# Kernel tuning notes

Measured on AMD Instinct MI355X. Metric: run time of the kernel, lower is better.

The kernel has to match this reference:

```python
import jax, jax.numpy as jnp
import numpy as np

SEQ_LEN = 256
VOCAB = 50000
EMBED = 300
PROJ = 200
ATT = 200
CLS = 3
B = 128


def setup_inputs() -> dict:
    key = jax.random.key(0)
    ks = jax.random.split(key, 16)
    s = lambda d: 1.0 / np.sqrt(d)
    return {
        "x1": jax.random.randint(ks[0], (B, SEQ_LEN), 0, VOCAB, dtype=jnp.int32),
        "x2": jax.random.randint(ks[1], (B, SEQ_LEN), 0, VOCAB, dtype=jnp.int32),
        "emb": jax.random.normal(ks[2], (VOCAB, EMBED), jnp.float32),
        # intra-attention forward_product FC (shared for x1/x2 via AUTO_REUSE)
        "Wi": jax.random.normal(ks[3], (EMBED, ATT), jnp.float32) * s(EMBED),
        "bi": jnp.zeros((ATT,), jnp.float32),
        "b_dist": jax.random.normal(ks[4], (1,), jnp.float32) * 0.1,
        # embed-scope projection (input is concat[x, xp] -> 2*EMBED), linear
        "Wp": jax.random.normal(ks[5], (2 * EMBED, PROJ), jnp.float32) * s(2 * EMBED),
        "bp": jnp.zeros((PROJ,), jnp.float32),
        # attent forward_product FC (shared)
        "Wa": jax.random.normal(ks[6], (PROJ, ATT), jnp.float32) * s(PROJ),
        "ba": jnp.zeros((ATT,), jnp.float32),
        # compare FC (shared, dim = input dim = 2*PROJ)
        "Wc": jax.random.normal(ks[7], (2 * PROJ, 2 * PROJ), jnp.float32) * s(2 * PROJ),
        "bc": jnp.zeros((2 * PROJ,), jnp.float32),
        # aggregate FC -> class logits (linear)
        "Wg": jax.random.normal(ks[8], (4 * PROJ, CLS), jnp.float32) * s(4 * PROJ),
        "bg": jnp.zeros((CLS,), jnp.float32),
    }


def _seq_mask(x):
    # tf.count_nonzero + tf.sequence_mask -> [B, L, 1] float mask
    size = jnp.sum((x != 0).astype(jnp.float32), axis=1)  # [B]
    m = (jnp.arange(SEQ_LEN)[None, :] < size[:, None]).astype(jnp.float32)
    return m[:, :, None]


def _intra(x, Wi, bi, b_dist):
    # forward_product on (x, x): relu FC then bilinear product -> [B, L, L]
    f = jax.nn.relu(x @ Wi + bi)
    att = jnp.einsum("bid,bjd->bij", f, f)
    idx = jnp.arange(SEQ_LEN)
    dist = jnp.abs(idx[None, :] - idx[:, None])
    bias = b_dist[0] * (dist >= 10).astype(jnp.float32)  # [L, L]
    xp = jnp.einsum("bik,bkj->bij", jax.nn.softmax(att + bias[None], axis=2), x)
    return jnp.concatenate([x, xp], axis=2)  # [B, L, 2*EMBED]


def reference(x1, x2, emb, Wi, bi, b_dist, Wp, bp, Wa, ba, Wc, bc, Wg, bg):
    mask1, mask2 = _seq_mask(x1), _seq_mask(x2)  # [B, L, 1]

    # embedding lookup with L2-normalized table
    emb_n = emb / jnp.linalg.norm(emb, axis=1, keepdims=True)
    e1, e2 = emb_n[x1], emb_n[x2]  # [B, L, EMBED]

    # intra-attention (distance-biased self alignment), doubles feature dim
    h1 = _intra(e1, Wi, bi, b_dist)
    h2 = _intra(e2, Wi, bi, b_dist)

    # linear projection to PROJ
    p1 = h1 @ Wp + bp  # [B, L, PROJ]
    p2 = h2 @ Wp + bp

    # attent: forward_product sim + mask + dual-axis softmax alignments
    a1 = jax.nn.relu(p1 @ Wa + ba)
    a2 = jax.nn.relu(p2 @ Wa + ba)
    sim = jnp.einsum("bid,bjd->bij", a1, a2)  # [B, L, L]
    sim = sim * (mask1 * jnp.swapaxes(mask2, 1, 2))
    alpha = jnp.einsum("bki,bkj->bij", jax.nn.softmax(sim, axis=1), p1)
    beta = jnp.einsum("bik,bkj->bij", jax.nn.softmax(sim, axis=2), p2)

    # compare (shared relu FC)
    v1 = jax.nn.relu(jnp.concatenate([p1, beta], 2) @ Wc + bc)
    v2 = jax.nn.relu(jnp.concatenate([p2, alpha], 2) @ Wc + bc)

    # aggregate: masked sum pooling + linear classifier
    v1 = jnp.sum(v1 * mask1, axis=1)  # [B, 2*PROJ]
    v2 = jnp.sum(v2 * mask2, axis=1)
    return jnp.concatenate([v1, v2], 1) @ Wg + bg  # [B, CLS]
```

## Files before the change

kernel.cpp:

```cpp
#include <hip/hip_runtime.h>
#include <math.h>

#define LSEQ 256
#define NB   128

typedef unsigned short u16;
typedef unsigned int   u32;
typedef __attribute__((ext_vector_type(8))) short bf16x8;
typedef __attribute__((ext_vector_type(4))) float f32x4;

static __device__ __forceinline__ u16 f2bf(float x) {
    union { float f; u32 u; } v; v.f = x;
    const u32 r = v.u + 0x7fffu + ((v.u >> 16) & 1u);
    return (u16)(r >> 16);
}
static __device__ __forceinline__ u32 cvt_pk(float lo, float hi) {
    u32 r; asm("v_cvt_pk_bf16_f32 %0, %1, %2" : "=v"(r) : "v"(lo), "v"(hi));
    return r;
}
static __device__ __forceinline__ u16 f2bf_fast(float x) {
    u32 r; asm("v_cvt_pk_bf16_f32 %0, %1, %1" : "=v"(r) : "v"(x));
    return (u16)r;
}
static __device__ __forceinline__ void glds16(const u16* src, u16* dst) {
    __builtin_amdgcn_global_load_lds(
        (const __attribute__((address_space(1))) u32*)src,
        (__attribute__((address_space(3))) u32*)dst, 16, 0, 0);
}
static __device__ __forceinline__ void bar_lgkm() {
    asm volatile("s_waitcnt lgkmcnt(0)" ::: "memory");
    __builtin_amdgcn_s_barrier();
}

template<int EPI, bool BIAS, bool RELU>
__global__ __launch_bounds__(512)
void gemm(const u16* __restrict__ A, int lda,
          const u16* __restrict__ B, int ldb,
          u16* __restrict__ C, int ldc,
          const float* __restrict__ bias, int Nbias,
          float* __restrict__ pool, const float* __restrict__ pmask,
          int K, int Nwrite)
{
    __shared__ u16 As[128 * 64];
    __shared__ u16 Bs[256 * 64];

    const int m0 = blockIdx.y * 128;
    const int n0 = blockIdx.x * 256;
    const int t = threadIdx.x;
    const int lane = t & 63;
    const int w = t >> 6;
    const int wm = w >> 2;
    const int wn = w & 3;
    const int lr = lane & 15;
    const int lg = lane >> 4;

    f32x4 acc[4][4] = {};

    for (int k0 = 0; k0 < K; k0 += 64) {
#pragma unroll
        for (int i = 0; i < 2; ++i) {
            const int ch = w * 2 + i;
            const int row = (ch << 3) + (lane >> 3);
            const int slot = (lane & 7) ^ (row & 7);
            glds16(A + (long long)(m0 + row) * lda + k0 + (slot << 3), &As[ch << 9]);
        }
#pragma unroll
        for (int i = 0; i < 4; ++i) {
            const int ch = w * 4 + i;
            const int row = (ch << 3) + (lane >> 3);
            const int slot = (lane & 7) ^ (row & 7);
            glds16(B + (long long)(n0 + row) * ldb + k0 + (slot << 3), &Bs[ch << 9]);
        }
        __syncthreads();
#pragma unroll
        for (int kk = 0; kk < 2; ++kk) {
            bf16x8 af[4], bf[4];
#pragma unroll
            for (int mi = 0; mi < 4; ++mi) {
                const int row = wm * 64 + mi * 16 + lr;
                const int slot = ((kk << 2) + lg) ^ (row & 7);
                af[mi] = *reinterpret_cast<const bf16x8*>(&As[row * 64 + (slot << 3)]);
            }
#pragma unroll
            for (int ni = 0; ni < 4; ++ni) {
                const int row = wn * 64 + ni * 16 + lr;
                const int slot = ((kk << 2) + lg) ^ (row & 7);
                bf[ni] = *reinterpret_cast<const bf16x8*>(&Bs[row * 64 + (slot << 3)]);
            }
#pragma unroll
            for (int mi = 0; mi < 4; ++mi)
#pragma unroll
                for (int ni = 0; ni < 4; ++ni)
                    acc[mi][ni] = __builtin_amdgcn_mfma_f32_16x16x32_bf16(
                        af[mi], bf[ni], acc[mi][ni], 0, 0, 0);
        }
        __syncthreads();
    }

    const int rbase = lg << 2;
    if (EPI == 0) {
#pragma unroll
        for (int ni = 0; ni < 4; ++ni) {
            const int gc = n0 + wn * 64 + ni * 16 + lr;
            if (gc >= Nwrite) continue;
            float bcv = 0.f;
            if (BIAS) bcv = (gc < Nbias) ? bias[gc] : 0.f;
#pragma unroll
            for (int mi = 0; mi < 4; ++mi) {
#pragma unroll
                for (int r = 0; r < 4; ++r) {
                    const long long gr = m0 + wm * 64 + mi * 16 + rbase + r;
                    float x = acc[mi][ni][r];
                    if (BIAS) x += bcv;
                    if (RELU) x = fmaxf(x, 0.f);
                    C[gr * ldc + gc] = f2bf_fast(x);
                }
            }
        }
    } else {
        __syncthreads();
        float* pool_s = reinterpret_cast<float*>(As);
        for (int i = t; i < 256; i += 512) pool_s[i] = 0.f;
        __syncthreads();
        const int b_lin = m0 >> 8;
        const int side  = b_lin >> 7;
        const int bb    = b_lin & 127;
        const float* mk = pmask + b_lin * 256 + (m0 & 255);
        float mrow[4][4];
#pragma unroll
        for (int mi = 0; mi < 4; ++mi)
#pragma unroll
            for (int r = 0; r < 4; ++r)
                mrow[mi][r] = mk[wm * 64 + mi * 16 + rbase + r];
#pragma unroll
        for (int ni = 0; ni < 4; ++ni) {
            const int lc = wn * 64 + ni * 16 + lr;
            const int gc = n0 + lc;
            const float bcv = (BIAS && gc < Nbias) ? bias[gc] : 0.f;
            float cs = 0.f;
#pragma unroll
            for (int mi = 0; mi < 4; ++mi)
#pragma unroll
                for (int r = 0; r < 4; ++r)
                    cs += fmaxf(acc[mi][ni][r] + bcv, 0.f) * mrow[mi][r];
            cs += __shfl_xor(cs, 16, 64);
            cs += __shfl_xor(cs, 32, 64);
            if (lg == 0) atomicAdd(&pool_s[lc], cs);
        }
        __syncthreads();
        for (int i = t; i < 256; i += 512) {
            const int gc = n0 + i;
            if (gc < Nwrite) atomicAdd(&pool[bb * 800 + side * 400 + gc], pool_s[i]);
        }
    }
}

template<int MODE>
__global__ __launch_bounds__(512)
void fattn(const u16* __restrict__ QK, u16* __restrict__ Hb,
           u16* __restrict__ CMP, u16* __restrict__ CMP2,
           const float* __restrict__ M1, const float* __restrict__ M2,
           const float* __restrict__ b_dist)
{
    constexpr int NVT = (MODE == 0) ? 5 : 4;
    __shared__ __align__(16) char shmem[MODE == 0 ? 57344 : 65536];
    u16* Pc = (u16*)shmem;
    u16* Vc = (u16*)(shmem + 16384);
    float* red  = (float*)shmem;
    float* red2 = red + 512;

    const int bz = blockIdx.x;
    int b, half, rowoff, ldv, ldc, Nwrite;
    const u16 *Kp, *Qp, *Vp;
    u16* Cp;
    const float *mrow = nullptr, *mcol = nullptr;
    if (MODE == 0) {
        b = (bz & 7) + (bz >> 4) * 8;
        half = (bz >> 3) & 1;
        Kp = QK + (long long)b * 65536;
        Qp = Kp;
        Vp = Hb + (long long)b * 163840; ldv = 640;
        Cp = Hb + (long long)b * 163840 + half * 128 * 640 + 320;
        ldc = 640; Nwrite = 320; rowoff = half * 128;
    } else {
        const int xcd = bz & 7, j = bz >> 3;
        const int sib = j & 3;
        b = xcd + (j >> 2) * 8;
        half = sib & 1;
        const int v = sib >> 1;
        const u16* a1 = QK + (long long)b * 65536;
        const u16* a2 = QK + 32768LL * 256 + (long long)b * 65536;
        u16* P1 = CMP  + (long long)b * 114688;
        u16* P2 = CMP2 + (long long)b * 114688;
        if (v == 0) { Qp = a1 + half * 128 * 256; Kp = a2; Vp = P2;
                      Cp = P1 + half * 128 * 448 + 200;
                      mrow = M1 + b * 256 + half * 128; mcol = M2 + b * 256; }
        else        { Qp = a2 + half * 128 * 256; Kp = a1; Vp = P1;
                      Cp = P2 + half * 128 * 448 + 200;
                      mrow = M2 + b * 256 + half * 128; mcol = M1 + b * 256; }
        ldv = 448; ldc = 448; Nwrite = 248; rowoff = 0;
    }

    const int t = threadIdx.x, lane = t & 63, w = t >> 6;
    const int lr = lane & 15, lg = lane >> 4;
    const int wk = w >> 1, wr = w & 1;
    const int wr2 = w >> 2, wc = w & 3;

    f32x4 acc[4][4] = {};
    {
        const int krow = lane >> 2;
        const int kslot = (lane & 3) ^ ((krow ^ (krow >> 2)) & 3);
        if (MODE != 0)
            glds16(Qp + (long long)(w * 16 + krow) * 256 + (kslot << 3),
                   (u16*)(shmem + 49152) + (w << 9));
#pragma unroll
        for (int i = 0; i < 2; ++i) {
            const int ch = w * 2 + i;
            glds16(Kp + (long long)(ch * 16 + krow) * 256 + (kslot << 3),
                   (u16*)shmem + (ch << 9));
        }
#pragma unroll
        for (int i = 0; i < 2; ++i) {
            const int ch = w * 2 + i;
            glds16(Kp + (long long)(ch * 16 + krow) * 256 + 32 + (kslot << 3),
                   (u16*)(shmem + 16384) + (ch << 9));
        }
#pragma unroll
        for (int it = 0; it < 8; ++it) {
            if (it == 7) asm volatile("s_waitcnt vmcnt(0)" ::: "memory");
            else         asm volatile("s_waitcnt vmcnt(2)" ::: "memory");
            __builtin_amdgcn_s_barrier();
            if (MODE != 0 && it < 7) {
                u16* qb2 = (u16*)(shmem + 49152 + (((it + 1) & 1) << 13));
                glds16(Qp + (long long)(w * 16 + krow) * 256 + (it + 1) * 32 + (kslot << 3),
                       qb2 + (w << 9));
            }
            if (it < 6) {
                u16* kb2 = (u16*)(shmem + ((it + 2) % 3) * 16384);
#pragma unroll
                for (int i = 0; i < 2; ++i) {
                    const int ch = w * 2 + i;
                    glds16(Kp + (long long)(ch * 16 + krow) * 256 + (it + 2) * 32 + (kslot << 3),
                           kb2 + (ch << 9));
                }
            }
            const u16* kb = (const u16*)(shmem + (it % 3) * 16384);
            const u16* qb = (MODE == 0) ? kb
                          : (const u16*)(shmem + 49152 + ((it & 1) << 13));
            bf16x8 kf[4], qf[4];
#pragma unroll
            for (int ki = 0; ki < 4; ++ki) {
                const int row = wk * 64 + ki * 16 + lr;
                const int phys = lg ^ ((row ^ (row >> 2)) & 3);
                kf[ki] = *reinterpret_cast<const bf16x8*>(&kb[row * 32 + (phys << 3)]);
            }
#pragma unroll
            for (int qi = 0; qi < 4; ++qi) {
                const int row = (MODE == 0 ? rowoff : 0) + wr * 64 + qi * 16 + lr;
                const int phys = lg ^ ((row ^ (row >> 2)) & 3);
                qf[qi] = *reinterpret_cast<const bf16x8*>(&qb[row * 32 + (phys << 3)]);
            }
            __builtin_amdgcn_s_setprio(1);
#pragma unroll
            for (int ki = 0; ki < 4; ++ki)
#pragma unroll
                for (int qi = 0; qi < 4; ++qi)
                    acc[ki][qi] = __builtin_amdgcn_mfma_f32_16x16x32_bf16(
                        kf[ki], qf[qi], acc[ki][qi], 0, 0, 0);
            __builtin_amdgcn_s_setprio(0);
        }
    }

    if (MODE == 1) {
        float mr[4], mc[4][4];
#pragma unroll
        for (int qi = 0; qi < 4; ++qi) mr[qi] = mrow[wr * 64 + qi * 16 + lr];
#pragma unroll
        for (int ki = 0; ki < 4; ++ki)
#pragma unroll
            for (int r = 0; r < 4; ++r)
                mc[ki][r] = mcol[wk * 64 + ki * 16 + (lg << 2) + r];
#pragma unroll
        for (int ki = 0; ki < 4; ++ki)
#pragma unroll
            for (int qi = 0; qi < 4; ++qi)
#pragma unroll
                for (int r = 0; r < 4; ++r)
                    acc[ki][qi][r] *= mr[qi] * mc[ki][r];
    } else {
        const float bd = b_dist[0];
#pragma unroll
        for (int ki = 0; ki < 4; ++ki) {
            const int kb_ = wk * 64 + ki * 16;
#pragma unroll
            for (int qi = 0; qi < 4; ++qi) {
                const int qb_ = rowoff + wr * 64 + qi * 16;
                const int diff = qb_ - kb_;
                if (diff >= -24 && diff <= 24) {
                    const int irow = qb_ + lr;
                    const int jc0  = kb_ + (lg << 2);
#pragma unroll
                    for (int r = 0; r < 4; ++r) {
                        const int d = irow - (jc0 + r);
                        const int ad = d < 0 ? -d : d;
                        if (ad < 10) acc[ki][qi][r] -= bd;
                    }
                }
            }
        }
    }

    const int n4  = (t & 63) << 2;
    const int k8v = (t >> 6) << 3;
    const int n4b = 256 + ((t & 15) << 2);
    const int k8b = (t >> 4) << 3;
    uint2 vreg[8], vtail[8];
#pragma unroll
    for (int i = 0; i < 8; ++i)
        vreg[i] = *reinterpret_cast<const uint2*>(Vp + (long long)(k8v + i) * ldv + n4);
    if (NVT == 5) {
        if (t < 128) {
#pragma unroll
            for (int i = 0; i < 8; ++i)
                vtail[i] = *reinterpret_cast<const uint2*>(Vp + (long long)(k8b + i) * ldv + n4b);
        }
    }

    float mx[4];
#pragma unroll
    for (int qi = 0; qi < 4; ++qi) {
        float m_ = -1e30f;
#pragma unroll
        for (int ki = 0; ki < 4; ++ki)
#pragma unroll
            for (int r = 0; r < 4; ++r) m_ = fmaxf(m_, acc[ki][qi][r]);
        m_ = fmaxf(m_, __shfl_xor(m_, 16, 64));
        m_ = fmaxf(m_, __shfl_xor(m_, 32, 64));
        mx[qi] = m_;
    }
    if (lg == 0) {
#pragma unroll
        for (int qi = 0; qi < 4; ++qi)
            red[(wr * 64 + qi * 16 + lr) * 4 + wk] = mx[qi];
    }
    bar_lgkm();
    float sm[4];
#pragma unroll
    for (int qi = 0; qi < 4; ++qi) {
        const int row = wr * 64 + qi * 16 + lr;
        const float m_ = fmaxf(fmaxf(red[row * 4 + 0], red[row * 4 + 1]),
                               fmaxf(red[row * 4 + 2], red[row * 4 + 3]));
        float s_ = 0.f;
#pragma unroll
        for (int ki = 0; ki < 4; ++ki)
#pragma unroll
            for (int r = 0; r < 4; ++r) {
                const float e_ = __expf(acc[ki][qi][r] - m_);
                acc[ki][qi][r] = e_;
                s_ += e_;
            }
        s_ += __shfl_xor(s_, 16, 64);
        s_ += __shfl_xor(s_, 32, 64);
        sm[qi] = s_;
    }
    if (lg == 0) {
#pragma unroll
        for (int qi = 0; qi < 4; ++qi)
            red2[(wr * 64 + qi * 16 + lr) * 4 + wk] = sm[qi];
    }
    bar_lgkm();
#pragma unroll
    for (int qi = 0; qi < 4; ++qi) {
        const int row = wr * 64 + qi * 16 + lr;
        const float rs = 1.0f / (red2[row * 4 + 0] + red2[row * 4 + 1]
                               + red2[row * 4 + 2] + red2[row * 4 + 3]);
#pragma unroll
        for (int ki = 0; ki < 4; ++ki)
#pragma unroll
            for (int r = 0; r < 4; ++r) acc[ki][qi][r] *= rs;
    }
    bar_lgkm();

    f32x4 opv[4][NVT] = {};
    for (int c = 0; c < 4; ++c) {
        {
            union { uint2 q2[8]; u16 s[32]; } uq;
#pragma unroll
            for (int i = 0; i < 8; ++i) uq.q2[i] = vreg[i];
#pragma unroll
            for (int j = 0; j < 4; ++j) {
                const int row = n4 + j;
                const u32 v0 = (u32)uq.s[j]      | ((u32)uq.s[4 + j]  << 16);
                const u32 v1 = (u32)uq.s[8 + j]  | ((u32)uq.s[12 + j] << 16);
                const u32 v2 = (u32)uq.s[16 + j] | ((u32)uq.s[20 + j] << 16);
                const u32 v3 = (u32)uq.s[24 + j] | ((u32)uq.s[28 + j] << 16);
                const int slot = (t >> 6) ^ (row & 7);
                *reinterpret_cast<uint4*>(&Vc[row * 64 + (slot << 3)]) =
                    make_uint4(v0, v1, v2, v3);
            }
            if (NVT == 5 && t < 128) {
                union { uint2 q2[8]; u16 s[32]; } ub;
#pragma unroll
                for (int i = 0; i < 8; ++i) ub.q2[i] = vtail[i];
#pragma unroll
                for (int j = 0; j < 4; ++j) {
                    const int row = n4b + j;
                    const u32 v0 = (u32)ub.s[j]      | ((u32)ub.s[4 + j]  << 16);
                    const u32 v1 = (u32)ub.s[8 + j]  | ((u32)ub.s[12 + j] << 16);
                    const u32 v2 = (u32)ub.s[16 + j] | ((u32)ub.s[20 + j] << 16);
                    const u32 v3 = (u32)ub.s[24 + j] | ((u32)ub.s[28 + j] << 16);
                    const int slot = (t >> 4) ^ (row & 7);
                    *reinterpret_cast<uint4*>(&Vc[row * 64 + (slot << 3)]) =
                        make_uint4(v0, v1, v2, v3);
                }
            }
        }
        if (wk == c) {
#pragma unroll
            for (int qi = 0; qi < 4; ++qi) {
                const int qrow = wr * 64 + qi * 16 + lr;
#pragma unroll
                for (int ki = 0; ki < 4; ++ki) {
                    const u32 lo = cvt_pk(acc[ki][qi][0], acc[ki][qi][1]);
                    const u32 hi = cvt_pk(acc[ki][qi][2], acc[ki][qi][3]);
                    const int slot = ((ki << 1) + (lg >> 1)) ^ (qrow & 7);
                    *reinterpret_cast<uint2*>(
                        (char*)Pc + qrow * 128 + (slot << 4) + ((lg & 1) << 3)) =
                        make_uint2(lo, hi);
                }
            }
        }
        if (c < 3) {
#pragma unroll
            for (int i = 0; i < 8; ++i)
                vreg[i] = *reinterpret_cast<const uint2*>(
                    Vp + (long long)((c + 1) * 64 + k8v + i) * ldv + n4);
            if (NVT == 5 && t < 128) {
#pragma unroll
                for (int i = 0; i < 8; ++i)
                    vtail[i] = *reinterpret_cast<const uint2*>(
                        Vp + (long long)((c + 1) * 64 + k8b + i) * ldv + n4b);
            }
        }
        bar_lgkm();
#pragma unroll
        for (int kk = 0; kk < 2; ++kk) {
            bf16x8 pa[4], vb[NVT];
#pragma unroll
            for (int qi = 0; qi < 4; ++qi) {
                const int row = wr2 * 64 + qi * 16 + lr;
                const int slot = ((kk << 2) + lg) ^ (row & 7);
                pa[qi] = *reinterpret_cast<const bf16x8*>(&Pc[row * 64 + (slot << 3)]);
            }
#pragma unroll
            for (int vi = 0; vi < NVT; ++vi) {
                const int row = wc * (NVT * 16) + vi * 16 + lr;
                const int slot = ((kk << 2) + lg) ^ (row & 7);
                vb[vi] = *reinterpret_cast<const bf16x8*>(&Vc[row * 64 + (slot << 3)]);
            }
            __builtin_amdgcn_s_setprio(1);
#pragma unroll
            for (int qi = 0; qi < 4; ++qi)
#pragma unroll
                for (int vi = 0; vi < NVT; ++vi)
                    opv[qi][vi] = __builtin_amdgcn_mfma_f32_16x16x32_bf16(
                        pa[qi], vb[vi], opv[qi][vi], 0, 0, 0);
            __builtin_amdgcn_s_setprio(0);
        }
        bar_lgkm();
    }

#pragma unroll
    for (int qi = 0; qi < 4; ++qi)
#pragma unroll
        for (int vi = 0; vi < NVT; ++vi) {
            const int gc = wc * (NVT * 16) + vi * 16 + lr;
            if (gc >= Nwrite) continue;
#pragma unroll
            for (int r = 0; r < 4; ++r) {
                const int qrow = wr2 * 64 + qi * 16 + (lg << 2) + r;
                Cp[(long long)qrow * ldc + gc] = f2bf_fast(opv[qi][vi][r]);
            }
        }
}

__global__ __launch_bounds__(256)
void prep_all(const int* __restrict__ x1, const int* __restrict__ x2,
              const float* __restrict__ emb,
              const float* __restrict__ Wi, const float* __restrict__ Wa,
              const float* __restrict__ Wp, const float* __restrict__ Wc,
              u16* __restrict__ h,
              u16* __restrict__ WiT, u16* __restrict__ WaT,
              u16* __restrict__ WpT, u16* __restrict__ WcT,
              float* __restrict__ M1f, float* __restrict__ POOL)
{
    const int blk = blockIdx.x;
    const int t = threadIdx.x;
    if (blk < 16384) {
        const int lane = t & 63;
        const long long row = (long long)blk * 4 + (t >> 6);
        const int tok = (row < 32768) ? x1[row] : x2[row - 32768];
        const float* er = emb + (long long)tok * 300;
        float vals[5];
        float ss = 0.f;
#pragma unroll
        for (int i = 0; i < 5; ++i) {
            const int c = lane + i * 64;
            const float v = (c < 300) ? er[c] : 0.f;
            vals[i] = v;
            ss = fmaf(v, v, ss);
        }
#pragma unroll
        for (int o = 32; o; o >>= 1) ss += __shfl_xor(ss, o, 64);
        const float inv = 1.0f / sqrtf(ss);
        u16* outp = h + row * 640;
#pragma unroll
        for (int i = 0; i < 5; ++i) {
            const int c = lane + i * 64;
            outp[c] = f2bf(vals[i] * inv);
        }
    } else if (blk < 18496) {
        int idx = (blk - 16384) * 256 + t;
        const float* src; u16* dst; int srcRows, srcCols, dstCols, seg1, seg2;
        if (idx < 81920)       { src = Wi; dst = WiT; srcRows = 300; srcCols = 200; dstCols = 320; seg1 = 300; seg2 = 320; }
        else if (idx < 147456) { idx -= 81920;  src = Wa; dst = WaT; srcRows = 200; srcCols = 200; dstCols = 256; seg1 = 200; seg2 = 256; }
        else if (idx < 311296) { idx -= 147456; src = Wp; dst = WpT; srcRows = 600; srcCols = 200; dstCols = 640; seg1 = 300; seg2 = 320; }
        else                   { idx -= 311296; src = Wc; dst = WcT; srcRows = 400; srcCols = 400; dstCols = 448; seg1 = 400; seg2 = 448; }
        const int n = idx / dstCols, k = idx - n * dstCols;
        int sr = -1;
        if (k < seg1) sr = k;
        else if (k >= seg2 && (k - seg2) < (srcRows - seg1)) sr = seg1 + (k - seg2);
        u16 v = 0;
        if (n < srcCols && sr >= 0) v = f2bf(src[(long long)sr * srcCols + n]);
        dst[idx] = v;
    } else {
        const int b2 = blk - 18496;
        const int b = b2 & 127;
        const int* x = (b2 < 128) ? x1 : x2;
        float* mask = M1f + (b2 < 128 ? 0 : 32768);
        int nz = (x[b * LSEQ + t] != 0) ? 1 : 0;
#pragma unroll
        for (int o = 32; o; o >>= 1) nz += __shfl_xor(nz, o, 64);
        __shared__ int red[4];
        if ((t & 63) == 0) red[t >> 6] = nz;
        __syncthreads();
        const int size = red[0] + red[1] + red[2] + red[3];
        mask[b * LSEQ + t] = (t < size) ? 1.0f : 0.0f;
        if (b2 < 128) {
            for (int i = t; i < 800; i += 256) POOL[b * 800 + i] = 0.f;
        }
    }
}

__global__ __launch_bounds__(256)
void final_fc(const float* __restrict__ pooled, const float* __restrict__ Wg,
              const float* __restrict__ bg, float* __restrict__ out)
{
    const int b = blockIdx.x;
    const int t = threadIdx.x;
    float a0 = 0.f, a1 = 0.f, a2 = 0.f;
    for (int k = t; k < 800; k += 256) {
        const float p = pooled[(long long)b * 800 + k];
        a0 = fmaf(p, Wg[k * 3 + 0], a0);
        a1 = fmaf(p, Wg[k * 3 + 1], a1);
        a2 = fmaf(p, Wg[k * 3 + 2], a2);
    }
#pragma unroll
    for (int o = 32; o; o >>= 1) {
        a0 += __shfl_xor(a0, o, 64);
        a1 += __shfl_xor(a1, o, 64);
        a2 += __shfl_xor(a2, o, 64);
    }
    __shared__ float r0[4], r1[4], r2[4];
    if ((t & 63) == 0) { r0[t >> 6] = a0; r1[t >> 6] = a1; r2[t >> 6] = a2; }
    __syncthreads();
    if (t == 0) {
        out[b * 3 + 0] = r0[0] + r0[1] + r0[2] + r0[3] + bg[0];
        out[b * 3 + 1] = r1[0] + r1[1] + r1[2] + r1[3] + bg[1];
        out[b * 3 + 2] = r2[0] + r2[1] + r2[2] + r2[3] + bg[2];
    }
}

extern "C" void kernel_launch(void* const* d_in, const int* in_sizes, int n_in,
                              void* d_out, int out_size, void* d_ws, size_t ws_size,
                              hipStream_t stream)
{
    (void)in_sizes; (void)n_in; (void)out_size; (void)ws_size;

    const int*   x1     = (const int*)  d_in[0];
    const int*   x2     = (const int*)  d_in[1];
    const float* emb    = (const float*)d_in[2];
    const float* Wi     = (const float*)d_in[3];
    const float* bi     = (const float*)d_in[4];
    const float* b_dist = (const float*)d_in[5];
    const float* Wp     = (const float*)d_in[6];
    const float* bp     = (const float*)d_in[7];
    const float* Wa     = (const float*)d_in[8];
    const float* ba     = (const float*)d_in[9];
    const float* Wc     = (const float*)d_in[10];
    const float* bc     = (const float*)d_in[11];
    const float* Wg     = (const float*)d_in[12];
    const float* bg     = (const float*)d_in[13];
    float* out = (float*)d_out;

    u16* wsu  = (u16*)d_ws;
    u16* H    = wsu;
    u16* CMP  = wsu + 41943040;
    u16* FA   = wsu + 71303168;
    u16* WiT  = wsu + 88080384;
    u16* WaT  = wsu + 88162304;
    u16* WpT  = wsu + 88227840;
    u16* WcT  = wsu + 88391680;
    float* fb = (float*)(wsu + 88621056);
    float* POOL = fb;
    float* M1f  = fb + 102400;
    float* M2f  = fb + 135168;

    u16* CMP2 = CMP + (long long)32768 * 448;

    prep_all<<<18752, 256, 0, stream>>>(x1, x2, emb, Wi, Wa, Wp, Wc,
                                        H, WiT, WaT, WpT, WcT, M1f, POOL);

    gemm<0, true, true><<<dim3(1, 512, 1), 512, 0, stream>>>(
        H, 640, WiT, 320, FA, 256, bi, 200, nullptr, nullptr, 320, 256);
    fattn<0><<<512, 512, 0, stream>>>(FA, H, nullptr, nullptr, nullptr, nullptr, b_dist);
    gemm<0, true, false><<<dim3(1, 512, 1), 512, 0, stream>>>(
        H, 640, WpT, 640, CMP, 448, bp, 200, nullptr, nullptr, 640, 256);
    gemm<0, true, true><<<dim3(1, 512, 1), 512, 0, stream>>>(
        CMP, 448, WaT, 256, FA, 256, ba, 200, nullptr, nullptr, 256, 256);
    fattn<1><<<512, 512, 0, stream>>>(FA, nullptr, CMP, CMP2, M1f, M2f, nullptr);
    gemm<2, true, true><<<dim3(2, 512, 1), 512, 0, stream>>>(
        CMP, 448, WcT, 448, nullptr, 0, bc, 400, POOL, M1f, 448, 400);

    final_fc<<<NB, 256, 0, stream>>>(POOL, Wg, bg, out);
}
```

Measured before the change: 196.7 us.

## Double-buffer GEMM with 256x256 tiles and interleaved async prefetch

Replaces the 128x256-tile GEMM with a 256x256-tile version that double-buffers A and B in 128KB of dynamic LDS. The loads for the next K-tile are issued between MFMA phases, gated by vmcnt waits and paired with setprio. This is meant to hide global-load latency behind compute and raise reuse of B fragments across twice as many rows. In exchange the grid is halved to 256 blocks, register pressure rises with 8x4 accumulators, and the large LDS footprint likely limits occupancy to one block per CU.

```diff
diff --git a/kernel.cpp b/kernel.cpp
--- a/kernel.cpp
+++ b/kernel.cpp
@@ -33,18 +33,17 @@
 }
 
 template<int EPI, bool BIAS, bool RELU>
-__global__ __launch_bounds__(512)
-void gemm(const u16* __restrict__ A, int lda,
-          const u16* __restrict__ B, int ldb,
-          u16* __restrict__ C, int ldc,
-          const float* __restrict__ bias, int Nbias,
-          float* __restrict__ pool, const float* __restrict__ pmask,
-          int K, int Nwrite)
+__global__ __launch_bounds__(512, 2)
+void gemm256(const u16* __restrict__ A, int lda,
+             const u16* __restrict__ B, int ldb,
+             u16* __restrict__ C, int ldc,
+             const float* __restrict__ bias, int Nbias,
+             float* __restrict__ pool, const float* __restrict__ pmask,
+             int K, int Nwrite)
 {
-    __shared__ u16 As[128 * 64];
-    __shared__ u16 Bs[256 * 64];
-
-    const int m0 = blockIdx.y * 128;
+    extern __shared__ u16 sm[];
+
+    const int m0 = blockIdx.y * 256;
     const int n0 = blockIdx.x * 256;
     const int t = threadIdx.x;
     const int lane = t & 63;
@@ -54,47 +53,99 @@
     const int lr = lane & 15;
     const int lg = lane >> 4;
 
-    f32x4 acc[4][4] = {};
-
-    for (int k0 = 0; k0 < K; k0 += 64) {
-#pragma unroll
-        for (int i = 0; i < 2; ++i) {
-            const int ch = w * 2 + i;
-            const int row = (ch << 3) + (lane >> 3);
-            const int slot = (lane & 7) ^ (row & 7);
-            glds16(A + (long long)(m0 + row) * lda + k0 + (slot << 3), &As[ch << 9]);
-        }
-#pragma unroll
-        for (int i = 0; i < 4; ++i) {
-            const int ch = w * 4 + i;
-            const int row = (ch << 3) + (lane >> 3);
-            const int slot = (lane & 7) ^ (row & 7);
-            glds16(B + (long long)(n0 + row) * ldb + k0 + (slot << 3), &Bs[ch << 9]);
-        }
-        __syncthreads();
-#pragma unroll
-        for (int kk = 0; kk < 2; ++kk) {
-            bf16x8 af[4], bf[4];
-#pragma unroll
-            for (int mi = 0; mi < 4; ++mi) {
-                const int row = wm * 64 + mi * 16 + lr;
-                const int slot = ((kk << 2) + lg) ^ (row & 7);
-                af[mi] = *reinterpret_cast<const bf16x8*>(&As[row * 64 + (slot << 3)]);
-            }
-#pragma unroll
-            for (int ni = 0; ni < 4; ++ni) {
+    const int nt = K >> 6;
+
+    auto stage = [&](int tt, int c) {
+        u16* base = sm + ((tt & 1) << 15);
+        const int koff = tt << 6;
+        if (c < 4) {
+            const int row = (c << 6) + (w << 3) + (lane >> 3);
+            const int ss = (lane & 7) ^ (row & 7);
+            glds16(B + (long long)(n0 + row) * ldb + koff + (ss << 3),
+                   base + 16384 + (((c << 6) + (w << 3)) << 6));
+        } else {
+            const int blk = (c == 4) ? 0 : (c == 5) ? 2 : (c == 6) ? 1 : 3;
+            const int row = (blk << 6) + (w << 3) + (lane >> 3);
+            const int ss = (lane & 7) ^ (row & 7);
+            glds16(A + (long long)(m0 + row) * lda + koff + (ss << 3),
+                   base + (((blk << 6) + (w << 3)) << 6));
+        }
+    };
+
+    f32x4 acc[8][4] = {};
+
+#pragma unroll
+    for (int c = 0; c < 8; ++c) stage(0, c);
+
+    for (int kt = 0; kt < nt; ++kt) {
+        const bool more = (kt + 1 < nt);
+        const u16* As = sm + ((kt & 1) << 15);
+        const u16* Bs = As + 16384;
+
+        asm volatile("s_waitcnt vmcnt(2)" ::: "memory");
+        __builtin_amdgcn_s_barrier();
+
+        bf16x8 bfr[4][2];
+#pragma unroll
+        for (int ni = 0; ni < 4; ++ni)
+#pragma unroll
+            for (int kk = 0; kk < 2; ++kk) {
                 const int row = wn * 64 + ni * 16 + lr;
-                const int slot = ((kk << 2) + lg) ^ (row & 7);
-                bf[ni] = *reinterpret_cast<const bf16x8*>(&Bs[row * 64 + (slot << 3)]);
-            }
-#pragma unroll
-            for (int mi = 0; mi < 4; ++mi)
+                const int ss = ((kk << 2) + lg) ^ (row & 7);
+                bfr[ni][kk] = *reinterpret_cast<const bf16x8*>(&Bs[row * 64 + (ss << 3)]);
+            }
+
+#pragma unroll
+        for (int ph = 0; ph < 2; ++ph) {
+            bf16x8 af[2][2];
+#pragma unroll
+            for (int i = 0; i < 2; ++i)
+#pragma unroll
+                for (int kk = 0; kk < 2; ++kk) {
+                    const int row = wm * 128 + (ph * 2 + i) * 16 + lr;
+                    const int ss = ((kk << 2) + lg) ^ (row & 7);
+                    af[i][kk] = *reinterpret_cast<const bf16x8*>(&As[row * 64 + (ss << 3)]);
+                }
+            if (more) { stage(kt + 1, ph * 2); stage(kt + 1, ph * 2 + 1); }
+            __builtin_amdgcn_s_setprio(1);
+#pragma unroll
+            for (int i = 0; i < 2; ++i)
 #pragma unroll
                 for (int ni = 0; ni < 4; ++ni)
-                    acc[mi][ni] = __builtin_amdgcn_mfma_f32_16x16x32_bf16(
-                        af[mi], bf[ni], acc[mi][ni], 0, 0, 0);
-        }
-        __syncthreads();
+#pragma unroll
+                    for (int kk = 0; kk < 2; ++kk)
+                        acc[ph * 2 + i][ni] = __builtin_amdgcn_mfma_f32_16x16x32_bf16(
+                            af[i][kk], bfr[ni][kk], acc[ph * 2 + i][ni], 0, 0, 0);
+            __builtin_amdgcn_s_setprio(0);
+        }
+
+        if (more) asm volatile("s_waitcnt vmcnt(4)" ::: "memory");
+        else      asm volatile("s_waitcnt vmcnt(0)" ::: "memory");
+        __builtin_amdgcn_s_barrier();
+
+#pragma unroll
+        for (int ph = 0; ph < 2; ++ph) {
+            bf16x8 af[2][2];
+#pragma unroll
+            for (int i = 0; i < 2; ++i)
+#pragma unroll
+                for (int kk = 0; kk < 2; ++kk) {
+                    const int row = wm * 128 + 64 + (ph * 2 + i) * 16 + lr;
+                    const int ss = ((kk << 2) + lg) ^ (row & 7);
+                    af[i][kk] = *reinterpret_cast<const bf16x8*>(&As[row * 64 + (ss << 3)]);
+                }
+            if (more) { stage(kt + 1, 4 + ph * 2); stage(kt + 1, 5 + ph * 2); }
+            __builtin_amdgcn_s_setprio(1);
+#pragma unroll
+            for (int i = 0; i < 2; ++i)
+#pragma unroll
+                for (int ni = 0; ni < 4; ++ni)
+#pragma unroll
+                    for (int kk = 0; kk < 2; ++kk)
+                        acc[4 + ph * 2 + i][ni] = __builtin_amdgcn_mfma_f32_16x16x32_bf16(
+                            af[i][kk], bfr[ni][kk], acc[4 + ph * 2 + i][ni], 0, 0, 0);
+            __builtin_amdgcn_s_setprio(0);
+        }
     }
 
     const int rbase = lg << 2;
@@ -106,10 +157,10 @@
             float bcv = 0.f;
             if (BIAS) bcv = (gc < Nbias) ? bias[gc] : 0.f;
 #pragma unroll
-            for (int mi = 0; mi < 4; ++mi) {
+            for (int mi = 0; mi < 8; ++mi) {
 #pragma unroll
                 for (int r = 0; r < 4; ++r) {
-                    const long long gr = m0 + wm * 64 + mi * 16 + rbase + r;
+                    const long long gr = m0 + wm * 128 + mi * 16 + rbase + r;
                     float x = acc[mi][ni][r];
                     if (BIAS) x += bcv;
                     if (RELU) x = fmaxf(x, 0.f);
@@ -119,19 +170,19 @@
         }
     } else {
         __syncthreads();
-        float* pool_s = reinterpret_cast<float*>(As);
+        float* pool_s = reinterpret_cast<float*>(sm);
         for (int i = t; i < 256; i += 512) pool_s[i] = 0.f;
         __syncthreads();
-        const int b_lin = m0 >> 8;
+        const int b_lin = blockIdx.y;
         const int side  = b_lin >> 7;
         const int bb    = b_lin & 127;
-        const float* mk = pmask + b_lin * 256 + (m0 & 255);
-        float mrow[4][4];
-#pragma unroll
-        for (int mi = 0; mi < 4; ++mi)
+        const float* mk = pmask + b_lin * 256;
+        float mrow[8][4];
+#pragma unroll
+        for (int mi = 0; mi < 8; ++mi)
 #pragma unroll
             for (int r = 0; r < 4; ++r)
-                mrow[mi][r] = mk[wm * 64 + mi * 16 + rbase + r];
+                mrow[mi][r] = mk[wm * 128 + mi * 16 + rbase + r];
 #pragma unroll
         for (int ni = 0; ni < 4; ++ni) {
             const int lc = wn * 64 + ni * 16 + lr;
@@ -139,7 +190,7 @@
             const float bcv = (BIAS && gc < Nbias) ? bias[gc] : 0.f;
             float cs = 0.f;
 #pragma unroll
-            for (int mi = 0; mi < 4; ++mi)
+            for (int mi = 0; mi < 8; ++mi)
 #pragma unroll
                 for (int r = 0; r < 4; ++r)
                     cs += fmaxf(acc[mi][ni][r] + bcv, 0.f) * mrow[mi][r];
@@ -344,7 +395,7 @@
             red[(wr * 64 + qi * 16 + lr) * 4 + wk] = mx[qi];
     }
     bar_lgkm();
-    float sm[4];
+    float sm_[4];
 #pragma unroll
     for (int qi = 0; qi < 4; ++qi) {
         const int row = wr * 64 + qi * 16 + lr;
@@ -361,12 +412,12 @@
             }
         s_ += __shfl_xor(s_, 16, 64);
         s_ += __shfl_xor(s_, 32, 64);
-        sm[qi] = s_;
+        sm_[qi] = s_;
     }
     if (lg == 0) {
 #pragma unroll
         for (int qi = 0; qi < 4; ++qi)
-            red2[(wr * 64 + qi * 16 + lr) * 4 + wk] = sm[qi];
+            red2[(wr * 64 + qi * 16 + lr) * 4 + wk] = sm_[qi];
     }
     bar_lgkm();
 #pragma unroll
@@ -603,6 +654,13 @@
     const float* bg     = (const float*)d_in[13];
     float* out = (float*)d_out;
 
+    hipFuncSetAttribute((const void*)&gemm256<0, true, true>,
+                        hipFuncAttributeMaxDynamicSharedMemorySize, 131072);
+    hipFuncSetAttribute((const void*)&gemm256<0, true, false>,
+                        hipFuncAttributeMaxDynamicSharedMemorySize, 131072);
+    hipFuncSetAttribute((const void*)&gemm256<2, true, true>,
+                        hipFuncAttributeMaxDynamicSharedMemorySize, 131072);
+
     u16* wsu  = (u16*)d_ws;
     u16* H    = wsu;
     u16* CMP  = wsu + 41943040;
@@ -621,15 +679,15 @@
     prep_all<<<18752, 256, 0, stream>>>(x1, x2, emb, Wi, Wa, Wp, Wc,
                                         H, WiT, WaT, WpT, WcT, M1f, POOL);
 
-    gemm<0, true, true><<<dim3(1, 512, 1), 512, 0, stream>>>(
+    gemm256<0, true, true><<<dim3(1, 256, 1), 512, 131072, stream>>>(
         H, 640, WiT, 320, FA, 256, bi, 200, nullptr, nullptr, 320, 256);
     fattn<0><<<512, 512, 0, stream>>>(FA, H, nullptr, nullptr, nullptr, nullptr, b_dist);
-    gemm<0, true, false><<<dim3(1, 512, 1), 512, 0, stream>>>(
+    gemm256<0, true, false><<<dim3(1, 256, 1), 512, 131072, stream>>>(
         H, 640, WpT, 640, CMP, 448, bp, 200, nullptr, nullptr, 640, 256);
-    gemm<0, true, true><<<dim3(1, 512, 1), 512, 0, stream>>>(
+    gemm256<0, true, true><<<dim3(1, 256, 1), 512, 131072, stream>>>(
         CMP, 448, WaT, 256, FA, 256, ba, 200, nullptr, nullptr, 256, 256);
     fattn<1><<<512, 512, 0, stream>>>(FA, nullptr, CMP, CMP2, M1f, M2f, nullptr);
-    gemm<2, true, true><<<dim3(2, 512, 1), 512, 0, stream>>>(
+    gemm256<2, true, true><<<dim3(2, 256, 1), 512, 131072, stream>>>(
         CMP, 448, WcT, 448, nullptr, 0, bc, 400, POOL, M1f, 448, 400);
 
     final_fc<<<NB, 256, 0, stream>>>(POOL, Wg, bg, out);
```

Result: no change. 199.3 us (+1.3%).
